# Kernel optimization log

Measured on AMD Instinct MI355X. Metric: run time of the kernel, lower is better.

## Reference

```python
import jax, jax.numpy as jnp
import numpy as np
import math

D_MODEL = 1024
N_HEADS = 16
D_HEAD = 64
D_MLP = 4096
N_LAYERS = 12
INIT_STD = 0.02
EPS = 1e-5
BATCH = 2
SEQ = 2048


def setup_inputs() -> dict:
    key = jax.random.key(0)
    ks = jax.random.split(key, 8)
    attn_std = INIT_STD
    proj_std = INIT_STD / math.sqrt(2 * N_LAYERS)
    return {
        "resid_pre": jax.random.normal(ks[0], (BATCH, SEQ, D_MODEL), jnp.float32),
        "ln1_w": jnp.ones((D_MODEL,), jnp.float32),
        "ln1_b": jnp.zeros((D_MODEL,), jnp.float32),
        "W_Q": attn_std * jax.random.normal(ks[1], (N_HEADS, D_MODEL, D_HEAD), jnp.float32),
        "b_Q": jnp.zeros((N_HEADS, D_HEAD), jnp.float32),
        "W_K": attn_std * jax.random.normal(ks[2], (N_HEADS, D_MODEL, D_HEAD), jnp.float32),
        "b_K": jnp.zeros((N_HEADS, D_HEAD), jnp.float32),
        "W_V": attn_std * jax.random.normal(ks[3], (N_HEADS, D_MODEL, D_HEAD), jnp.float32),
        "b_V": jnp.zeros((N_HEADS, D_HEAD), jnp.float32),
        "W_O": proj_std * jax.random.normal(ks[4], (N_HEADS, D_HEAD, D_MODEL), jnp.float32),
        "b_O": jnp.zeros((D_MODEL,), jnp.float32),
        "ln2_w": jnp.ones((D_MODEL,), jnp.float32),
        "ln2_b": jnp.zeros((D_MODEL,), jnp.float32),
        "W_in": INIT_STD * jax.random.normal(ks[5], (D_MODEL, D_MLP), jnp.float32),
        "b_in": jnp.zeros((D_MLP,), jnp.float32),
        "W_out": proj_std * jax.random.normal(ks[6], (D_MLP, D_MODEL), jnp.float32),
        "b_out": jnp.zeros((D_MODEL,), jnp.float32),
    }


def _layernorm(x, w, b):
    mean = x.mean(-1, keepdims=True)
    var = x.var(-1, keepdims=True)  # unbiased=False
    return (x - mean) / jnp.sqrt(var + EPS) * w + b


def _attention(x, W_Q, b_Q, W_K, b_K, W_V, b_V, W_O, b_O):
    # x: [b, s, d]; W_*: [h, d, k]
    q = jnp.einsum('bsd,hdk->bshk', x, W_Q) + b_Q
    k = jnp.einsum('bsd,hdk->bshk', x, W_K) + b_K
    v = jnp.einsum('bsd,hdk->bshk', x, W_V) + b_V
    scores = jnp.einsum('bqhk,bshk->bhqs', q, k) / math.sqrt(D_HEAD)
    seq = x.shape[1]
    causal = jnp.tril(jnp.ones((seq, seq), bool))
    scores = jnp.where(causal, scores, -jnp.inf)
    pattern = jax.nn.softmax(scores, axis=-1)
    z = jnp.einsum('bhqs,bshk->bqhk', pattern, v)
    return jnp.einsum('bqhk,hkd->bqd', z, W_O) + b_O


def reference(resid_pre, ln1_w, ln1_b, W_Q, b_Q, W_K, b_K, W_V, b_V, W_O, b_O,
              ln2_w, ln2_b, W_in, b_in, W_out, b_out):
    attn_out = _attention(_layernorm(resid_pre, ln1_w, ln1_b),
                          W_Q, b_Q, W_K, b_K, W_V, b_V, W_O, b_O)
    resid_mid = resid_pre + attn_out
    h = _layernorm(resid_mid, ln2_w, ln2_b)
    mlp_out = jnp.matmul(jax.nn.relu(jnp.matmul(h, W_in) + b_in), W_out) + b_out
    return resid_mid + mlp_out
```

## Files before the change

kernel.cpp:

```cpp
#include <hip/hip_runtime.h>
#include <stdint.h>


typedef unsigned short u16;
typedef __bf16 bf16x8 __attribute__((ext_vector_type(8)));
typedef __bf16 bf16x4 __attribute__((ext_vector_type(4)));
typedef __bf16 bf16x2 __attribute__((ext_vector_type(2)));
typedef short  s16x4  __attribute__((ext_vector_type(4)));
typedef float  f32x4  __attribute__((ext_vector_type(4)));

#define QSCALE 0.18033688011112042f

__device__ __forceinline__ float bf2f(unsigned int u) {
  union { unsigned int u; float f; } v; v.u = u << 16; return v.f;
}
__device__ __forceinline__ u16 f2bf(float f) {
  union { float f; unsigned int u; } v; v.f = f;
  unsigned int r = v.u + 0x7FFFu + ((v.u >> 16) & 1u);
  return (u16)(r >> 16);
}
__device__ __forceinline__ unsigned pkbf(float lo, float hi) {
#if __has_builtin(__builtin_amdgcn_cvt_pk_bf16_f32)
  bf16x2 t = __builtin_amdgcn_cvt_pk_bf16_f32(lo, hi);
  return __builtin_bit_cast(unsigned, t);
#else
  return (unsigned)f2bf(lo) | ((unsigned)f2bf(hi) << 16);
#endif
}
__device__ __forceinline__ float loadf(const void* p, size_t i, int isf) {
  return isf ? ((const float*)p)[i] : bf2f(((const u16*)p)[i]);
}

__device__ __forceinline__ f32x4 mfma16(s16x4 a, s16x4 b, f32x4 c) {
#if __has_builtin(__builtin_amdgcn_mfma_f32_16x16x16_bf16)
  return __builtin_amdgcn_mfma_f32_16x16x16_bf16(
      __builtin_bit_cast(bf16x4, a), __builtin_bit_cast(bf16x4, b), c, 0, 0, 0);
#else
  return __builtin_amdgcn_mfma_f32_16x16x16bf16_1k(a, b, c, 0, 0, 0);
#endif
}

__global__ __launch_bounds__(256) void detect_dtype(
    const unsigned int* __restrict__ x, int* __restrict__ flag) {
  __shared__ int cnt;
  if (threadIdx.x == 0) cnt = 0;
  __syncthreads();
  int c = 0;
  for (int i = threadIdx.x; i < 512; i += 256) {
    unsigned int e = (x[i] >> 23) & 0xFFu;
    if (e >= 97u && e <= 157u) c++;
  }
  atomicAdd(&cnt, c);
  __syncthreads();
  if (threadIdx.x == 0) *flag = (cnt > 384) ? 1 : 0;
}

__global__ __launch_bounds__(256) void pack_qkv_tiled(
    const int* __restrict__ flagp,
    const void* __restrict__ Wq, const void* __restrict__ Wk, const void* __restrict__ Wv,
    u16* __restrict__ WT) {
  __shared__ float t[64][65];
  const int isf = *flagp;
  const int tid = threadIdx.x;
  const int mh = blockIdx.y;
  const int mat = mh >> 4, h = mh & 15;
  const int d0 = blockIdx.x << 6;
  const void* src = (mat == 0) ? Wq : (mat == 1) ? Wk : Wv;
  const float scale = (mat == 0) ? QSCALE : 1.f;
  const int lane = tid & 63, rr = tid >> 6;
  const size_t sbase = ((size_t)h << 16) + lane;
#pragma unroll
  for (int i = 0; i < 16; i++) {
    int d = i * 4 + rr;
    t[d][lane] = loadf(src, sbase + (size_t)(d0 + d) * 64, isf) * scale;
  }
  __syncthreads();
#pragma unroll
  for (int i = 0; i < 16; i++) {
    int k = i * 4 + rr;
    WT[((size_t)((mat << 10) + (h << 6) + k) << 10) + d0 + lane] = f2bf(t[lane][k]);
  }
}

__global__ __launch_bounds__(256) void transpose_tiled(
    const int* __restrict__ flagp, const void* __restrict__ src,
    u16* __restrict__ dst, int R, int C) {
  __shared__ float t[64][65];
  const int isf = *flagp;
  const int tid = threadIdx.x;
  const int c0 = blockIdx.x << 6, r0 = blockIdx.y << 6;
  const int lane = tid & 63, rr = tid >> 6;
#pragma unroll
  for (int i = 0; i < 16; i++) {
    int r = i * 4 + rr;
    t[r][lane] = loadf(src, (size_t)(r0 + r) * C + c0 + lane, isf);
  }
  __syncthreads();
#pragma unroll
  for (int i = 0; i < 16; i++) {
    int c = i * 4 + rr;
    dst[(size_t)(c0 + c) * R + r0 + lane] = f2bf(t[lane][c]);
  }
}

__global__ __launch_bounds__(256) void pack_biases(
    const int* __restrict__ flagp,
    const void* bq, const void* bk, const void* bv,
    const void* bO, const void* bin, const void* bout,
    float* __restrict__ out) {
  const int isf = *flagp;
  int i = blockIdx.x * 256 + threadIdx.x;
  float v;
  if (i < 1024)      v = loadf(bq,   i,        isf) * QSCALE;
  else if (i < 2048) v = loadf(bk,   i - 1024, isf);
  else if (i < 3072) v = loadf(bv,   i - 2048, isf);
  else if (i < 4096) v = loadf(bO,   i - 3072, isf);
  else if (i < 8192) v = loadf(bin,  i - 4096, isf);
  else               v = loadf(bout, i - 8192, isf);
  out[i] = v;
}

template<int SRC>
__global__ __launch_bounds__(256) void ln_fwd(
    const int* __restrict__ flagp, const void* __restrict__ xin,
    const void* __restrict__ w, const void* __restrict__ b,
    u16* __restrict__ out) {
  const int isf = *flagp;
  const int row = blockIdx.x, tid = threadIdx.x;
  const int col = tid << 2;
  const size_t base = ((size_t)row << 10) + col;
  float v[4];
#pragma unroll
  for (int i = 0; i < 4; i++)
    v[i] = (SRC == 1) ? ((const float*)xin)[base + i] : loadf(xin, base + i, isf);
  float s  = v[0] + v[1] + v[2] + v[3];
  float ss = v[0]*v[0] + v[1]*v[1] + v[2]*v[2] + v[3]*v[3];
#pragma unroll
  for (int mk = 32; mk >= 1; mk >>= 1) {
    s  += __shfl_xor(s,  mk, 64);
    ss += __shfl_xor(ss, mk, 64);
  }
  __shared__ float red[8];
  if ((tid & 63) == 0) { red[tid >> 6] = s; red[4 + (tid >> 6)] = ss; }
  __syncthreads();
  float S  = red[0] + red[1] + red[2] + red[3];
  float SS = red[4] + red[5] + red[6] + red[7];
  float mean = S * (1.f / 1024.f);
  float var  = SS * (1.f / 1024.f) - mean * mean;
  float rstd = rsqrtf(var + 1e-5f);
  u16 e[4];
#pragma unroll
  for (int i = 0; i < 4; i++) {
    float wv = loadf(w, col + i, isf);
    float bv = loadf(b, col + i, isf);
    e[i] = f2bf((v[i] - mean) * rstd * wv + bv);
  }
  uint2 o;
  o.x = (unsigned)e[0] | ((unsigned)e[1] << 16);
  o.y = (unsigned)e[2] | ((unsigned)e[3] << 16);
  *(uint2*)(out + base) = o;
}

template<int MODE, int TM, int KW>
__global__ __launch_bounds__(KW * 256) void gemm_bt(
    const int* __restrict__ flagp,
    const u16* __restrict__ A, const u16* __restrict__ BT,
    const float* __restrict__ bias, const void* __restrict__ resid,
    void* __restrict__ out, void* __restrict__ out2, void* __restrict__ out3,
    int M, int N, int K, int SHL) {
  constexpr int WR = TM / 32;
  constexpr int ASZ = TM * 32;
  constexpr int BSZ = 128 * 32;
  constexpr int STAGE_B = KW * (ASZ + BSZ) * 2;
  constexpr int RED_B = (KW > 1) ? TM * 132 * 4 : 1;
  constexpr int SMEM_B = STAGE_B > RED_B ? STAGE_B : RED_B;
  __shared__ __align__(16) char smem[SMEM_B];
  u16* as = (u16*)smem;
  u16* bs = (u16*)smem + KW * ASZ;

  int isf = 0;
  if (MODE == 2 || MODE == 3) isf = *flagp;
  const int Lb = blockIdx.x;
  const int xcd = Lb & 7, sidx = Lb >> 3;
  const int SH = 1 << SHL;
  const int by = xcd * SH + (sidx & (SH - 1));
  const int bx = sidx >> SHL;
  const int tid = threadIdx.x;
  const int L = tid & 63, w = tid >> 6;
  const int g = w >> 2, wl = w & 3;
  const int wm = (wl >> 1) * (TM >> 1), wn = (wl & 1) << 6;
  const int row0 = by * TM, col0 = bx << 7;
  const int m = L & 15, quad = L >> 4;

  f32x4 zero4 = {0.f, 0.f, 0.f, 0.f};
  f32x4 acc[WR][4];
#pragma unroll
  for (int i = 0; i < WR; i++)
#pragma unroll
    for (int j = 0; j < 4; j++) acc[i][j] = zero4;

  const int KSEG = K / KW;
  const int tl = tid & 255;
  const int tm = tl >> 2;
  const int tk = (tl & 3) << 3;
  const u16* Ag  = A  + (size_t)(row0 + tm) * K + g * KSEG + tk;
  const u16* Ag2 = Ag + (size_t)64 * K;
  const u16* Bg  = BT + (size_t)(col0 + tm) * K + g * KSEG + tk;
  const u16* Bg2 = Bg + (size_t)64 * K;
  u16* asg  = as + g * ASZ;
  u16* bsg  = bs + g * BSZ;
  u16* asl  = asg + tl * 8;
  u16* asl2 = asg + 2048 + tl * 8;
  u16* bsl  = bsg + tl * 8;
  u16* bsl2 = bsg + 2048 + tl * 8;

  const int aoff = (wm + m) * 32 + quad * 8;
  const int boff = (wn + m) * 32 + quad * 8;

  int4 ar0, ar1, br0, br1;
  ar0 = *(const int4*)Ag;
  if (TM == 128) ar1 = *(const int4*)Ag2;
  br0 = *(const int4*)Bg;
  br1 = *(const int4*)Bg2;

  for (int kk = 0; kk < KSEG; kk += 32) {
    __syncthreads();
    *(int4*)asl = ar0;
    if (TM == 128) *(int4*)asl2 = ar1;
    *(int4*)bsl = br0;
    *(int4*)bsl2 = br1;
    __syncthreads();
    if (kk + 32 < KSEG) {
      ar0 = *(const int4*)(Ag + kk + 32);
      if (TM == 128) ar1 = *(const int4*)(Ag2 + kk + 32);
      br0 = *(const int4*)(Bg + kk + 32);
      br1 = *(const int4*)(Bg2 + kk + 32);
    }
    bf16x8 af[WR], bfr[4];
#pragma unroll
    for (int i = 0; i < WR; i++) af[i]  = *(const bf16x8*)&asg[aoff + i * 512];
#pragma unroll
    for (int j = 0; j < 4; j++) bfr[j] = *(const bf16x8*)&bsg[boff + j * 512];
#pragma unroll
    for (int i = 0; i < WR; i++)
#pragma unroll
      for (int j = 0; j < 4; j++)
        acc[i][j] = __builtin_amdgcn_mfma_f32_16x16x32_bf16(af[i], bfr[j], acc[i][j], 0, 0, 0);
  }

  if (KW > 1) {
    __syncthreads();
    float* red = (float*)smem;
    if (g == 1) {
#pragma unroll
      for (int i = 0; i < WR; i++)
#pragma unroll
        for (int j = 0; j < 4; j++)
#pragma unroll
          for (int r = 0; r < 4; r++)
            red[(wm + i * 16 + quad * 4 + r) * 132 + wn + j * 16 + m] = acc[i][j][r];
    }
    __syncthreads();
    if (g == 0) {
#pragma unroll
      for (int i = 0; i < WR; i++)
#pragma unroll
        for (int j = 0; j < 4; j++)
#pragma unroll
          for (int r = 0; r < 4; r++)
            acc[i][j][r] += red[(wm + i * 16 + quad * 4 + r) * 132 + wn + j * 16 + m];
    }
  }

  if (g == 0) {
#pragma unroll
    for (int j = 0; j < 4; j++) {
      const int col = col0 + wn + j * 16 + m;
      const float bval = bias[col];
      if (MODE == 4) {
        const int sel = col >> 10;
        const int hh  = (col >> 6) & 15;
        const int f   = col & 63;
#pragma unroll
        for (int i = 0; i < WR; i++) {
          const int rowb = row0 + wm + i * 16 + quad * 4;
          if (sel < 2) {
            u16* dst = (u16*)(sel ? out2 : out);
#pragma unroll
            for (int r = 0; r < 4; r++)
              dst[((((size_t)hh << 12) + rowb + r) << 6) + f] = f2bf(acc[i][j][r] + bval);
          } else {
            uint2 o;
            o.x = pkbf(acc[i][j][0] + bval, acc[i][j][1] + bval);
            o.y = pkbf(acc[i][j][2] + bval, acc[i][j][3] + bval);
            *(uint2*)&((u16*)out3)[(((size_t)hh * 64 + f) << 12) + rowb] = o;
          }
        }
      } else {
#pragma unroll
        for (int i = 0; i < WR; i++) {
          const int rowb = row0 + wm + i * 16 + quad * 4;
#pragma unroll
          for (int r = 0; r < 4; r++) {
            float vv = acc[i][j][r] + bval;
            size_t idx = (size_t)(rowb + r) * N + col;
            if (MODE == 1) {
              ((u16*)out)[idx] = f2bf(fmaxf(vv, 0.f));
            } else if (MODE == 2) {
              ((float*)out)[idx] = vv + loadf(resid, idx, isf);
            } else if (MODE == 3) {
              float o = vv + ((const float*)resid)[idx];
              if (isf) ((float*)out)[idx] = o;
              else     ((u16*)out)[idx]   = f2bf(o);
            }
          }
        }
      }
    }
  }
}

__global__ __launch_bounds__(512, 6) void attn_part(
    const u16* __restrict__ qh, const u16* __restrict__ kh,
    const u16* __restrict__ vT, u16* __restrict__ Opart,
    float* __restrict__ stats, u16* __restrict__ z) {
  const int combo = blockIdx.x;
  const int qt = blockIdx.y;
  const int ci = blockIdx.z;
  const int q0 = qt << 7;
  const int nc = (q0 + 128 + 1023) >> 10;
  if (ci >= nc) return;
  const int k_lo = ci << 10;
  const int k_hi = min(k_lo + 1024, q0 + 128);
  const int nsteps = (k_hi - k_lo + 127) >> 7;

  __shared__ u16 kS[128 * 72];
  __shared__ u16 vS[64 * 136];
  const int tid = threadIdx.x, L = tid & 63, w = tid >> 6;
  const int m = L & 15, quad = L >> 4;
  const int h = combo >> 1, b = combo & 1;
  const size_t tb = (size_t)b * 2048;
  const size_t hbase = (size_t)h * 4096;
  const int qg = q0 + w * 16 + m;

  bf16x8 qb0, qb1;
  {
    const u16* qp = qh + ((hbase + tb + (size_t)qg) << 6) + quad * 8;
    qb0 = *(const bf16x8*)qp;
    qb1 = *(const bf16x8*)(qp + 32);
  }

  f32x4 zero4 = {0.f, 0.f, 0.f, 0.f};
  f32x4 O[4];
#pragma unroll
  for (int ft = 0; ft < 4; ft++) O[ft] = zero4;
  float mrow = -30000.f, lrow = 0.f;

  const int krow[2] = { (0*512+tid) >> 3, (1*512+tid) >> 3 };
  const int kc = tid & 7;
  const int vf[2] = { (0*512+tid) >> 4, (1*512+tid) >> 4 };
  const int vc = tid & 15;
  const int vq = (vc & 1) << 1;
  const int vk4 = (vc >> 1) << 2;
  const int vc0 = (vq << 5) + vk4;
  const int vc1 = ((vq + 1) << 5) + vk4;

  int4 kr[2], vr[2];
#pragma unroll
  for (int i = 0; i < 2; i++) {
    kr[i] = *(const int4*)(kh + ((hbase + tb + k_lo + krow[i]) << 6) + kc * 8);
    vr[i] = *(const int4*)(vT + (((size_t)h * 64 + vf[i]) << 12) + tb + k_lo + vc * 8);
  }

  for (int j = 0; j < nsteps; j++) {
    const int k0 = k_lo + (j << 7);
    __syncthreads();
#pragma unroll
    for (int i = 0; i < 2; i++) {
      *(int4*)&kS[krow[i] * 72 + kc * 8] = kr[i];
      union { int4 v; s16x4 hh[2]; } tv; tv.v = vr[i];
      *(s16x4*)&vS[vf[i] * 136 + vc0] = tv.hh[0];
      *(s16x4*)&vS[vf[i] * 136 + vc1] = tv.hh[1];
    }
    __syncthreads();
    if (j + 1 < nsteps) {
      const int k1 = k_lo + ((j + 1) << 7);
#pragma unroll
      for (int i = 0; i < 2; i++) {
        kr[i] = *(const int4*)(kh + ((hbase + tb + k1 + krow[i]) << 6) + kc * 8);
        vr[i] = *(const int4*)(vT + (((size_t)h * 64 + vf[i]) << 12) + tb + k1 + vc * 8);
      }
    }
    f32x4 sc[8];
#pragma unroll
    for (int kt = 0; kt < 8; kt++) {
      const u16* kp = &kS[(kt * 16 + m) * 72 + quad * 8];
      bf16x8 ka0 = *(const bf16x8*)kp;
      bf16x8 ka1 = *(const bf16x8*)(kp + 32);
      f32x4 t = zero4;
      t = __builtin_amdgcn_mfma_f32_16x16x32_bf16(ka0, qb0, t, 0, 0, 0);
      t = __builtin_amdgcn_mfma_f32_16x16x32_bf16(ka1, qb1, t, 0, 0, 0);
      sc[kt] = t;
    }
    if (k0 + 128 > q0) {
#pragma unroll
      for (int kt = 0; kt < 8; kt++)
#pragma unroll
        for (int r = 0; r < 4; r++) {
          int ktok = k0 + kt * 16 + quad * 4 + r;
          if (ktok > qg) sc[kt][r] = -30000.f;
        }
    }
    float mx = sc[0][0];
#pragma unroll
    for (int kt = 0; kt < 8; kt++)
#pragma unroll
      for (int r = 0; r < 4; r++) mx = fmaxf(mx, sc[kt][r]);
    mx = fmaxf(mx, __shfl_xor(mx, 16, 64));
    mx = fmaxf(mx, __shfl_xor(mx, 32, 64));
    if (!__all(mx <= mrow + 8.f)) {
      float mnew = fmaxf(mrow, mx);
      float alpha = __builtin_amdgcn_exp2f(mrow - mnew);
      lrow *= alpha;
#pragma unroll
      for (int ft = 0; ft < 4; ft++) O[ft] *= alpha;
      mrow = mnew;
    }
    s16x4 pb[8];
    float sum = 0.f;
#pragma unroll
    for (int kt = 0; kt < 8; kt++) {
      float e0 = __builtin_amdgcn_exp2f(sc[kt][0] - mrow);
      float e1 = __builtin_amdgcn_exp2f(sc[kt][1] - mrow);
      float e2 = __builtin_amdgcn_exp2f(sc[kt][2] - mrow);
      float e3 = __builtin_amdgcn_exp2f(sc[kt][3] - mrow);
      sum += (e0 + e1) + (e2 + e3);
      union { uint2 u; s16x4 hh; } pu;
      pu.u.x = pkbf(e0, e1);
      pu.u.y = pkbf(e2, e3);
      pb[kt] = pu.hh;
    }
    sum += __shfl_xor(sum, 16, 64);
    sum += __shfl_xor(sum, 32, 64);
    lrow += sum;
#pragma unroll
    for (int ft = 0; ft < 4; ft++) {
      const u16* vp = &vS[(ft * 16 + m) * 136 + quad * 32];
#pragma unroll
      for (int pr = 0; pr < 4; pr++) {
        union { bf16x8 v; s16x4 hh[2]; } u;
        u.v = *(const bf16x8*)(vp + pr * 8);
        O[ft] = mfma16(u.hh[0], pb[2 * pr],     O[ft]);
        O[ft] = mfma16(u.hh[1], pb[2 * pr + 1], O[ft]);
      }
    }
  }

  if (nc == 1) {
    float inv = 1.f / lrow;
#pragma unroll
    for (int ft = 0; ft < 4; ft++) O[ft] *= inv;
  }

  __syncthreads();
#pragma unroll
  for (int ft = 0; ft < 4; ft++) {
    union { uint2 u; s16x4 hh; } o4;
    o4.u.x = pkbf(O[ft][0], O[ft][1]);
    o4.u.y = pkbf(O[ft][2], O[ft][3]);
    *(s16x4*)&kS[(w * 16 + m) * 72 + ft * 16 + quad * 4] = o4.hh;
  }
  __syncthreads();
  if (nc == 1) {
    u16* zp = z + ((tb + (size_t)q0) << 10) + h * 64;
#pragma unroll
    for (int it = 0; it < 2; it++) {
      int idx = it * 512 + tid;
      int row = idx >> 3, c = idx & 7;
      *(int4*)&zp[((size_t)row << 10) + c * 8] = *(const int4*)&kS[row * 72 + c * 8];
    }
  } else {
    const int slot = (combo * 16 + qt) * 2 + ci;
    u16* op = Opart + ((size_t)slot << 13);
#pragma unroll
    for (int it = 0; it < 2; it++) {
      int idx = it * 512 + tid;
      int row = idx >> 3, c = idx & 7;
      *(int4*)&op[row * 64 + c * 8] = *(const int4*)&kS[row * 72 + c * 8];
    }
    if (quad == 0) {
      stats[slot * 256 + w * 16 + m]       = mrow;
      stats[slot * 256 + 128 + w * 16 + m] = lrow;
    }
  }
}

__global__ __launch_bounds__(512) void attn_merge(
    const u16* __restrict__ Opart, const float* __restrict__ stats,
    u16* __restrict__ z) {
  const int combo = blockIdx.x, qt = 8 + blockIdx.y;
  const int h = combo >> 1, b = combo & 1;
  const int q0 = qt << 7;
  const int tid = threadIdx.x;
  const int t = tid >> 2, f0 = (tid & 3) << 4;
  const int slot0 = (combo * 16 + qt) * 2;
  float M = fmaxf(stats[slot0 * 256 + t], stats[(slot0 + 1) * 256 + t]);
  float acc[16];
#pragma unroll
  for (int e = 0; e < 16; e++) acc[e] = 0.f;
  float ltot = 0.f;
#pragma unroll
  for (int ci = 0; ci < 2; ci++) {
    float mi = stats[(slot0 + ci) * 256 + t];
    float li = stats[(slot0 + ci) * 256 + 128 + t];
    float wgt = exp2f(mi - M);
    ltot += wgt * li;
    const u16* op = Opart + (((size_t)(slot0 + ci)) << 13) + t * 64 + f0;
    union { int4 v; u16 u[8]; } a0, a1;
    a0.v = *(const int4*)op;
    a1.v = *(const int4*)(op + 8);
#pragma unroll
    for (int e = 0; e < 8; e++) {
      acc[e]     += wgt * bf2f(a0.u[e]);
      acc[8 + e] += wgt * bf2f(a1.u[e]);
    }
  }
  float inv = 1.f / ltot;
  union { int4 v; u16 u[8]; } o0, o1;
#pragma unroll
  for (int e = 0; e < 8; e++) {
    o0.u[e] = f2bf(acc[e] * inv);
    o1.u[e] = f2bf(acc[8 + e] * inv);
  }
  size_t tok = (size_t)b * 2048 + q0 + t;
  *(int4*)&z[tok * 1024 + h * 64 + f0]     = o0.v;
  *(int4*)&z[tok * 1024 + h * 64 + f0 + 8] = o1.v;
}

extern "C" void kernel_launch(void* const* d_in, const int* in_sizes, int n_in,
                              void* d_out, int out_size, void* d_ws, size_t ws_size,
                              hipStream_t stream) {
  (void)in_sizes; (void)n_in; (void)out_size; (void)ws_size;
  const void* resid_pre = d_in[0];
  const void* ln1_w = d_in[1];
  const void* ln1_b = d_in[2];
  const void* W_Q   = d_in[3];
  const void* b_Q   = d_in[4];
  const void* W_K   = d_in[5];
  const void* b_K   = d_in[6];
  const void* W_V   = d_in[7];
  const void* b_V   = d_in[8];
  const void* W_O   = d_in[9];
  const void* b_O   = d_in[10];
  const void* ln2_w = d_in[11];
  const void* ln2_b = d_in[12];
  const void* W_in  = d_in[13];
  const void* b_in  = d_in[14];
  const void* W_out = d_in[15];
  const void* b_out = d_in[16];

  char* p = (char*)d_ws;
  auto alloc = [&](size_t bytes) {
    char* r = p; p += (bytes + 255) & ~(size_t)255; return (void*)r;
  };
  int*   flag      = (int*)  alloc(256);
  u16*   WqkvT     = (u16*)  alloc(3072ull * 1024 * 2);
  u16*   WoT       = (u16*)  alloc(1024ull * 1024 * 2);
  u16*   WinT      = (u16*)  alloc(4096ull * 1024 * 2);
  u16*   WoutT     = (u16*)  alloc(1024ull * 4096 * 2);
  float* biases    = (float*)alloc(9216 * 4);
  u16*   xn        = (u16*)  alloc(4096ull * 1024 * 2);
  u16*   q_hm      = (u16*)  alloc(16ull * 4096 * 64 * 2);
  u16*   k_hm      = (u16*)  alloc(16ull * 4096 * 64 * 2);
  u16*   vTws      = (u16*)  alloc(16ull * 64 * 4096 * 2);
  float* resid_mid = (float*)alloc(4096ull * 1024 * 4);
  u16*   h2        = (u16*)  alloc(4096ull * 1024 * 2);
  u16*   act       = (u16*)  alloc(4096ull * 4096 * 2);
  u16*   z = xn;
  u16*   Opart = act;
  float* stats = (float*)h2;

  detect_dtype<<<1, 256, 0, stream>>>((const unsigned int*)resid_pre, flag);

  pack_qkv_tiled<<<dim3(16, 48), 256, 0, stream>>>(flag, W_Q, W_K, W_V, WqkvT);
  transpose_tiled<<<dim3(16, 16), 256, 0, stream>>>(flag, W_O,   WoT,   1024, 1024);
  transpose_tiled<<<dim3(64, 16), 256, 0, stream>>>(flag, W_in,  WinT,  1024, 4096);
  transpose_tiled<<<dim3(16, 64), 256, 0, stream>>>(flag, W_out, WoutT, 4096, 1024);
  pack_biases<<<36, 256, 0, stream>>>(flag, b_Q, b_K, b_V, b_O, b_in, b_out, biases);

  ln_fwd<0><<<4096, 256, 0, stream>>>(flag, resid_pre, ln1_w, ln1_b, xn);
  gemm_bt<4, 128, 1><<<768, 256, 0, stream>>>(
      flag, xn, WqkvT, biases, nullptr, q_hm, k_hm, vTws, 4096, 3072, 1024, 2);
  attn_part<<<dim3(32, 16, 2), 512, 0, stream>>>(q_hm, k_hm, vTws, Opart, stats, z);
  attn_merge<<<dim3(32, 8), 512, 0, stream>>>(Opart, stats, z);
  gemm_bt<2, 64, 2><<<512, 512, 0, stream>>>(
      flag, z, WoT, biases + 3072, resid_pre, resid_mid, nullptr, nullptr, 4096, 1024, 1024, 3);
  ln_fwd<1><<<4096, 256, 0, stream>>>(flag, resid_mid, ln2_w, ln2_b, h2);
  gemm_bt<1, 128, 1><<<1024, 256, 0, stream>>>(
      flag, h2, WinT, biases + 4096, nullptr, act, nullptr, nullptr, 4096, 4096, 1024, 2);
  gemm_bt<3, 64, 2><<<512, 512, 0, stream>>>(
      flag, act, WoutT, biases + 8192, resid_mid, d_out, nullptr, nullptr, 4096, 1024, 4096, 3);
}
```

Baseline: 453.8 us.

## Cut attention register pressure: split KV tile into halves, drop prefetch, raise occupancy

Measured after the change: 438.7 us. 3.3% less time.

```diff
diff --git a/kernel.cpp b/kernel.cpp
--- a/kernel.cpp
+++ b/kernel.cpp
@@ -320,7 +320,7 @@
   }
 }
 
-__global__ __launch_bounds__(512, 6) void attn_part(
+__global__ __launch_bounds__(512, 8) void attn_part(
     const u16* __restrict__ qh, const u16* __restrict__ kh,
     const u16* __restrict__ vT, u16* __restrict__ Opart,
     float* __restrict__ stats, u16* __restrict__ z) {
@@ -365,15 +365,14 @@
   const int vc0 = (vq << 5) + vk4;
   const int vc1 = ((vq + 1) << 5) + vk4;
 
-  int4 kr[2], vr[2];
-#pragma unroll
-  for (int i = 0; i < 2; i++) {
-    kr[i] = *(const int4*)(kh + ((hbase + tb + k_lo + krow[i]) << 6) + kc * 8);
-    vr[i] = *(const int4*)(vT + (((size_t)h * 64 + vf[i]) << 12) + tb + k_lo + vc * 8);
-  }
-
   for (int j = 0; j < nsteps; j++) {
     const int k0 = k_lo + (j << 7);
+    int4 kr[2], vr[2];
+#pragma unroll
+    for (int i = 0; i < 2; i++) {
+      kr[i] = *(const int4*)(kh + ((hbase + tb + k0 + krow[i]) << 6) + kc * 8);
+      vr[i] = *(const int4*)(vT + (((size_t)h * 64 + vf[i]) << 12) + tb + k0 + vc * 8);
+    }
     __syncthreads();
 #pragma unroll
     for (int i = 0; i < 2; i++) {
@@ -383,75 +382,73 @@
       *(s16x4*)&vS[vf[i] * 136 + vc1] = tv.hh[1];
     }
     __syncthreads();
-    if (j + 1 < nsteps) {
-      const int k1 = k_lo + ((j + 1) << 7);
-#pragma unroll
-      for (int i = 0; i < 2; i++) {
-        kr[i] = *(const int4*)(kh + ((hbase + tb + k1 + krow[i]) << 6) + kc * 8);
-        vr[i] = *(const int4*)(vT + (((size_t)h * 64 + vf[i]) << 12) + tb + k1 + vc * 8);
+
+#pragma unroll
+    for (int hs = 0; hs < 2; hs++) {
+      const int kbase = k0 + hs * 64;
+      f32x4 sc[4];
+#pragma unroll
+      for (int kt4 = 0; kt4 < 4; kt4++) {
+        const int kt = hs * 4 + kt4;
+        const u16* kp = &kS[(kt * 16 + m) * 72 + quad * 8];
+        bf16x8 ka0 = *(const bf16x8*)kp;
+        bf16x8 ka1 = *(const bf16x8*)(kp + 32);
+        f32x4 t = zero4;
+        t = __builtin_amdgcn_mfma_f32_16x16x32_bf16(ka0, qb0, t, 0, 0, 0);
+        t = __builtin_amdgcn_mfma_f32_16x16x32_bf16(ka1, qb1, t, 0, 0, 0);
+        sc[kt4] = t;
       }
-    }
-    f32x4 sc[8];
-#pragma unroll
-    for (int kt = 0; kt < 8; kt++) {
-      const u16* kp = &kS[(kt * 16 + m) * 72 + quad * 8];
-      bf16x8 ka0 = *(const bf16x8*)kp;
-      bf16x8 ka1 = *(const bf16x8*)(kp + 32);
-      f32x4 t = zero4;
-      t = __builtin_amdgcn_mfma_f32_16x16x32_bf16(ka0, qb0, t, 0, 0, 0);
-      t = __builtin_amdgcn_mfma_f32_16x16x32_bf16(ka1, qb1, t, 0, 0, 0);
-      sc[kt] = t;
-    }
-    if (k0 + 128 > q0) {
-#pragma unroll
-      for (int kt = 0; kt < 8; kt++)
-#pragma unroll
-        for (int r = 0; r < 4; r++) {
-          int ktok = k0 + kt * 16 + quad * 4 + r;
-          if (ktok > qg) sc[kt][r] = -30000.f;
+      if (kbase + 64 > q0) {
+#pragma unroll
+        for (int kt4 = 0; kt4 < 4; kt4++)
+#pragma unroll
+          for (int r = 0; r < 4; r++) {
+            int ktok = kbase + kt4 * 16 + quad * 4 + r;
+            if (ktok > qg) sc[kt4][r] = -30000.f;
+          }
+      }
+      float mx = sc[0][0];
+#pragma unroll
+      for (int kt4 = 0; kt4 < 4; kt4++)
+#pragma unroll
+        for (int r = 0; r < 4; r++) mx = fmaxf(mx, sc[kt4][r]);
+      mx = fmaxf(mx, __shfl_xor(mx, 16, 64));
+      mx = fmaxf(mx, __shfl_xor(mx, 32, 64));
+      if (!__all(mx <= mrow + 8.f)) {
+        float mnew = fmaxf(mrow, mx);
+        float alpha = __builtin_amdgcn_exp2f(mrow - mnew);
+        lrow *= alpha;
+#pragma unroll
+        for (int ft = 0; ft < 4; ft++) O[ft] *= alpha;
+        mrow = mnew;
+      }
+      s16x4 pb[4];
+      float sum = 0.f;
+#pragma unroll
+      for (int kt4 = 0; kt4 < 4; kt4++) {
+        float e0 = __builtin_amdgcn_exp2f(sc[kt4][0] - mrow);
+        float e1 = __builtin_amdgcn_exp2f(sc[kt4][1] - mrow);
+        float e2 = __builtin_amdgcn_exp2f(sc[kt4][2] - mrow);
+        float e3 = __builtin_amdgcn_exp2f(sc[kt4][3] - mrow);
+        sum += (e0 + e1) + (e2 + e3);
+        union { uint2 u; s16x4 hh; } pu;
+        pu.u.x = pkbf(e0, e1);
+        pu.u.y = pkbf(e2, e3);
+        pb[kt4] = pu.hh;
+      }
+      sum += __shfl_xor(sum, 16, 64);
+      sum += __shfl_xor(sum, 32, 64);
+      lrow += sum;
+#pragma unroll
+      for (int ft = 0; ft < 4; ft++) {
+        const u16* vp = &vS[(ft * 16 + m) * 136 + quad * 32 + hs * 16];
+#pragma unroll
+        for (int p2 = 0; p2 < 2; p2++) {
+          union { bf16x8 v; s16x4 hh[2]; } u;
+          u.v = *(const bf16x8*)(vp + p2 * 8);
+          O[ft] = mfma16(u.hh[0], pb[2 * p2],     O[ft]);
+          O[ft] = mfma16(u.hh[1], pb[2 * p2 + 1], O[ft]);
         }
-    }
-    float mx = sc[0][0];
-#pragma unroll
-    for (int kt = 0; kt < 8; kt++)
-#pragma unroll
-      for (int r = 0; r < 4; r++) mx = fmaxf(mx, sc[kt][r]);
-    mx = fmaxf(mx, __shfl_xor(mx, 16, 64));
-    mx = fmaxf(mx, __shfl_xor(mx, 32, 64));
-    if (!__all(mx <= mrow + 8.f)) {
-      float mnew = fmaxf(mrow, mx);
-      float alpha = __builtin_amdgcn_exp2f(mrow - mnew);
-      lrow *= alpha;
-#pragma unroll
-      for (int ft = 0; ft < 4; ft++) O[ft] *= alpha;
-      mrow = mnew;
-    }
-    s16x4 pb[8];
-    float sum = 0.f;
-#pragma unroll
-    for (int kt = 0; kt < 8; kt++) {
-      float e0 = __builtin_amdgcn_exp2f(sc[kt][0] - mrow);
-      float e1 = __builtin_amdgcn_exp2f(sc[kt][1] - mrow);
-      float e2 = __builtin_amdgcn_exp2f(sc[kt][2] - mrow);
-      float e3 = __builtin_amdgcn_exp2f(sc[kt][3] - mrow);
-      sum += (e0 + e1) + (e2 + e3);
-      union { uint2 u; s16x4 hh; } pu;
-      pu.u.x = pkbf(e0, e1);
-      pu.u.y = pkbf(e2, e3);
-      pb[kt] = pu.hh;
-    }
-    sum += __shfl_xor(sum, 16, 64);
-    sum += __shfl_xor(sum, 32, 64);
-    lrow += sum;
-#pragma unroll
-    for (int ft = 0; ft < 4; ft++) {
-      const u16* vp = &vS[(ft * 16 + m) * 136 + quad * 32];
-#pragma unroll
-      for (int pr = 0; pr < 4; pr++) {
-        union { bf16x8 v; s16x4 hh[2]; } u;
-        u.v = *(const bf16x8*)(vp + pr * 8);
-        O[ft] = mfma16(u.hh[0], pb[2 * pr],     O[ft]);
-        O[ft] = mfma16(u.hh[1], pb[2 * pr + 1], O[ft]);
       }
     }
   }
```
